# Optimization experiments

Hardware: AMD Instinct MI355X
Metric: run time of the kernel (lower is better)

Reference implementation:

```python
import jax, jax.numpy as jnp
import numpy as np

D_MODEL = 1024
N_HEADS = 16
D_FF = 2 * D_MODEL
EPS = 1e-6


def setup_inputs() -> dict:
    key = jax.random.key(0)
    ks = jax.random.split(key, 12)
    B, S, D = 2, 2048, D_MODEL
    w = lambda k, shape: (jax.random.normal(k, shape, dtype=jnp.float32) * 0.02)
    return {
        "x": jax.random.normal(ks[0], (B, S, D), dtype=jnp.float32),
        "mask": jnp.ones((B, S, S), dtype=jnp.int32),
        "alpha1": jnp.ones((D,), jnp.float32),
        "bias1": jnp.zeros((D,), jnp.float32),
        "Wq": w(ks[1], (D, D)), "bq": jnp.zeros((D,), jnp.float32),
        "Wk": w(ks[2], (D, D)), "bk": jnp.zeros((D,), jnp.float32),
        "Wv": w(ks[3], (D, D)), "bv": jnp.zeros((D,), jnp.float32),
        "Wo": w(ks[4], (D, D)), "bo": jnp.zeros((D,), jnp.float32),
        "alpha2": jnp.ones((D,), jnp.float32),
        "bias2": jnp.zeros((D,), jnp.float32),
        "W1": w(ks[5], (D, D_FF)), "b1": jnp.zeros((D_FF,), jnp.float32),
        "W2": w(ks[6], (D_FF, D)), "b2": jnp.zeros((D,), jnp.float32),
    }


def _norm(x, alpha, bias):
    # torch: alpha*(x-mean)/(std+eps)+bias, std is unbiased (ddof=1)
    mu = jnp.mean(x, axis=-1, keepdims=True)
    sd = jnp.std(x, axis=-1, ddof=1, keepdims=True)
    return alpha * (x - mu) / (sd + EPS) + bias


def _gelu(x):
    return jax.nn.gelu(x, approximate=False)  # torch F.gelu exact


def _attention(x2, mask, Wq, bq, Wk, bk, Wv, bv, Wo, bo):
    B, S, D = x2.shape
    h, dk = N_HEADS, D // N_HEADS
    # project and split heads: [B, h, S, dk]
    q = (x2 @ Wq + bq).reshape(B, S, h, dk).transpose(0, 2, 1, 3)
    k = (x2 @ Wk + bk).reshape(B, S, h, dk).transpose(0, 2, 1, 3)
    v = (x2 @ Wv + bv).reshape(B, S, h, dk).transpose(0, 2, 1, 3)
    scores = jnp.einsum('bhqd,bhkd->bhqk', q, k) / np.sqrt(dk).astype(np.float32)
    scores = jnp.where(mask[:, None] == 0, jnp.float32(-1e9), scores)
    attn = jax.nn.softmax(scores, axis=-1)
    out = jnp.einsum('bhqk,bhkd->bhqd', attn, v)
    out = out.transpose(0, 2, 1, 3).reshape(B, S, D)
    return out @ Wo + bo


def reference(x, mask, alpha1, bias1, Wq, bq, Wk, bk, Wv, bv, Wo, bo,
              alpha2, bias2, W1, b1, W2, b2):
    x2 = _norm(x, alpha1, bias1)
    x = x + _attention(x2, mask, Wq, bq, Wk, bk, Wv, bv, Wo, bo)
    x2 = _norm(x, alpha2, bias2)
    ff = _gelu(_gelu(x2 @ W1 + b1) @ W2 + b2)
    return x + ff
```

## Files before the change

### kernel.cpp

```cpp
#include <hip/hip_runtime.h>
#include <math.h>

typedef __attribute__((ext_vector_type(8))) short v8s;
typedef __attribute__((ext_vector_type(4))) float v4f;
typedef __attribute__((ext_vector_type(4))) unsigned int v4u;
typedef __attribute__((ext_vector_type(2))) unsigned int v2u;

#define MFMA16(a,b,c) __builtin_amdgcn_mfma_f32_16x16x32_bf16(a,b,c,0,0,0)
#define QSCALE 0.18033688011112042f

typedef const __attribute__((address_space(1))) void* gp1_t;
typedef __attribute__((address_space(3))) void* lp3_t;
__device__ __forceinline__ void gll16(const void* g, void* l){
  __builtin_amdgcn_global_load_lds((gp1_t)g, (lp3_t)l, 16, 0, 0);
}
#define VMCNT(n) asm volatile("s_waitcnt vmcnt(" #n ")" ::: "memory")

__device__ __forceinline__ unsigned short f2b(float f){
  unsigned u = __builtin_bit_cast(unsigned, f);
  u += 0x7FFFu + ((u>>16)&1u);
  return (unsigned short)(u>>16);
}
__device__ __forceinline__ unsigned cvtpk(float lo, float hi){
  unsigned r;
  asm("v_cvt_pk_bf16_f32 %0, %1, %2" : "=v"(r) : "v"(lo), "v"(hi));
  return r;
}
__device__ __forceinline__ float gelu_exact(float x){
  return 0.5f*x*(1.0f + erff(x*0.70710678118654752f));
}

__global__ __launch_bounds__(256) void ln_kernel(const float* __restrict__ x,
    const float* __restrict__ alpha, const float* __restrict__ bias,
    unsigned short* __restrict__ out)
{
  const int D = 1024;
  int row = blockIdx.x;
  int tid = threadIdx.x;
  const float* xr = x + (size_t)row*D;
  v4f v = ((const v4f*)xr)[tid];
  float s  = v[0]+v[1]+v[2]+v[3];
  float s2 = v[0]*v[0]+v[1]*v[1]+v[2]*v[2]+v[3]*v[3];
  #pragma unroll
  for (int off=1; off<64; off<<=1){ s += __shfl_xor(s, off); s2 += __shfl_xor(s2, off); }
  __shared__ float red[8];
  int w = tid>>6;
  if ((tid&63)==0){ red[w]=s; red[4+w]=s2; }
  __syncthreads();
  s  = red[0]+red[1]+red[2]+red[3];
  s2 = red[4]+red[5]+red[6]+red[7];
  float mu  = s*(1.0f/D);
  float var = (s2 - (float)D*mu*mu)*(1.0f/(D-1));
  float inv = 1.0f/(sqrtf(fmaxf(var,0.0f)) + 1e-6f);
  v4f a  = ((const v4f*)alpha)[tid];
  v4f bi = ((const v4f*)bias)[tid];
  unsigned short o[4];
  #pragma unroll
  for (int i=0;i<4;i++) o[i] = f2b(a[i]*(v[i]-mu)*inv + bi[i]);
  v2u pk; pk[0] = (unsigned)o[0] | ((unsigned)o[1]<<16);
          pk[1] = (unsigned)o[2] | ((unsigned)o[3]<<16);
  ((v2u*)(out + (size_t)row*D))[tid] = pk;
}

__global__ __launch_bounds__(256) void transpose_f2b(const float* __restrict__ in,
    unsigned short* __restrict__ out, int K, int N)
{
  __shared__ float t[32][33];
  int n0 = blockIdx.x*32, k0 = blockIdx.y*32;
  int tx = threadIdx.x, ty = threadIdx.y;
  #pragma unroll
  for (int j=0;j<4;j++) t[ty+8*j][tx] = in[(size_t)(k0+ty+8*j)*N + n0+tx];
  __syncthreads();
  #pragma unroll
  for (int j=0;j<4;j++) out[(size_t)(n0+ty+8*j)*K + k0+tx] = f2b(t[tx][ty+8*j]);
}

__global__ __launch_bounds__(256) void mask_flags(const int* __restrict__ mask,
    unsigned char* __restrict__ flags)
{
  const int S = 2048;
  int bid = blockIdx.x;
  int kt = bid & 31, qt = (bid>>5)&31, b = bid>>10;
  int tid = threadIdx.x;
  const int* mp = mask + (size_t)b*S*S + (size_t)(qt*64)*S + kt*64;
  int ok = 1;
  #pragma unroll
  for (int i=0;i<16;i++){
    int idx = tid + i*256;
    int row = idx>>6, col = idx&63;
    ok &= (mp[(size_t)row*S + col] != 0);
  }
  ok = __all(ok) ? 1 : 0;
  __shared__ int f[4];
  if ((tid&63)==0) f[tid>>6] = ok;
  __syncthreads();
  if (tid==0) flags[bid] = (unsigned char)(f[0]&f[1]&f[2]&f[3]);
}

__global__ __launch_bounds__(256) void v_transpose(const unsigned short* __restrict__ vB,
    unsigned short* __restrict__ vT)
{
  __shared__ unsigned short ts[64][68];
  int tt = blockIdx.x & 31, bh = blockIdx.x >> 5;
  int b = bh >> 4, h = bh & 15;
  int tid = threadIdx.x;
  int row = tid>>3, c8 = (tid&7)*8;
  const unsigned short* src = vB + ((size_t)(b*2048 + tt*64))*1024 + h*64;
  #pragma unroll
  for (int j=0;j<2;j++)
    *(v4u*)&ts[row+32*j][c8] = *(const v4u*)(src + (size_t)(row+32*j)*1024 + c8);
  __syncthreads();
  unsigned short* dst = vT + ((size_t)bh*64)*2048 + (size_t)tt*64;
  #pragma unroll
  for (int j=0;j<2;j++){
    int d = row + 32*j;
    unsigned short tmp[8];
    #pragma unroll
    for (int jj=0;jj<8;jj++) tmp[jj] = ts[c8+jj][d];
    *(v4u*)&dst[(size_t)d*2048 + c8] = *(const v4u*)tmp;
  }
}

__global__ __launch_bounds__(256) void gemm_qkv(
    const unsigned short* __restrict__ A, const unsigned short* __restrict__ Bt,
    const float* __restrict__ bq, const float* __restrict__ bk, const float* __restrict__ bv,
    unsigned short* __restrict__ qB, unsigned short* __restrict__ kB, unsigned short* __restrict__ vB)
{
  const int K = 1024, N = 1024;
  __shared__ unsigned short As[3][128][32];
  __shared__ unsigned short Bs[3][128][32];
  int m0 = blockIdx.x*128;
  int ny = blockIdx.y;
  int seg = ny>>3;
  int n0g = ny*128;
  int tid = threadIdx.x;
  int w = tid>>6, l = tid&63;
  int wm = (w>>1)*64, wn = (w&1)*64;
  int r16 = l&15, kq = l>>4;
  v4f acc[4][4] = {};
  int t4 = tid>>2, c8 = (tid&3)*8;
  const unsigned short* Ag = A  + (size_t)(m0 + t4)*K + c8;
  const unsigned short* Bg = Bt + (size_t)(n0g + t4)*K + c8;
  auto stageG = [&](int kb, int idx){
    char* a = (char*)&As[idx][0][0] + w*1024;
    char* b = (char*)&Bs[idx][0][0] + w*1024;
    gll16(Ag + kb,                a);
    gll16(Ag + (size_t)64*K + kb, a + 4096);
    gll16(Bg + kb,                b);
    gll16(Bg + (size_t)64*K + kb, b + 4096);
  };
  const int nk = K/32;
  stageG(0, 0); stageG(32, 1);
  for (int i=0; i<nk; i++){
    int cur = i%3;
    if (i+1 < nk) VMCNT(4); else VMCNT(0);
    __builtin_amdgcn_s_barrier();
    if (i+2 < nk) stageG((i+2)*32, (i+2)%3);
    v8s a[4], b[4];
    #pragma unroll
    for (int mi=0;mi<4;mi++) a[mi] = *(const v8s*)&As[cur][wm+mi*16+r16][kq*8];
    #pragma unroll
    for (int ni=0;ni<4;ni++) b[ni] = *(const v8s*)&Bs[cur][wn+ni*16+r16][kq*8];
    #pragma unroll
    for (int mi=0;mi<4;mi++)
      #pragma unroll
      for (int ni=0;ni<4;ni++)
        acc[mi][ni] = MFMA16(a[mi], b[ni], acc[mi][ni]);
  }
  unsigned short* ob = (seg==0) ? qB : (seg==1) ? kB : vB;
  const float*    bp = (seg==0) ? bq : (seg==1) ? bk : bv;
  float sc = (seg==0) ? QSCALE : 1.0f;
  int ncol0 = (ny&7)*128;
  #pragma unroll
  for (int mi=0;mi<4;mi++){
    #pragma unroll
    for (int ni=0;ni<4;ni++){
      int col = ncol0 + wn + ni*16 + r16;
      float bvv = bp[col];
      #pragma unroll
      for (int r=0;r<4;r++){
        int row = m0 + wm + mi*16 + kq*4 + r;
        ob[(size_t)row*N + col] = f2b((acc[mi][ni][r] + bvv)*sc);
      }
    }
  }
}

template<int MODE>
__global__ __launch_bounds__(256) void gemm_bt(
    const unsigned short* __restrict__ A, const unsigned short* __restrict__ Bt,
    const float* __restrict__ bias, const float* __restrict__ res,
    unsigned short* __restrict__ outb, float* __restrict__ outf,
    int M, int N, int K)
{
  __shared__ unsigned short As[3][128][32];
  __shared__ unsigned short Bs[3][128][32];
  int m0 = blockIdx.x*128, n0 = blockIdx.y*128;
  int tid = threadIdx.x;
  int w = tid>>6, l = tid&63;
  int wm = (w>>1)*64, wn = (w&1)*64;
  int r16 = l&15, kq = l>>4;
  v4f acc[4][4] = {};
  int t4 = tid>>2, c8 = (tid&3)*8;
  const unsigned short* Ag = A  + (size_t)(m0 + t4)*K + c8;
  const unsigned short* Bg = Bt + (size_t)(n0 + t4)*K + c8;
  auto stageG = [&](int kb, int idx){
    char* a = (char*)&As[idx][0][0] + w*1024;
    char* b = (char*)&Bs[idx][0][0] + w*1024;
    gll16(Ag + kb,                a);
    gll16(Ag + (size_t)64*K + kb, a + 4096);
    gll16(Bg + kb,                b);
    gll16(Bg + (size_t)64*K + kb, b + 4096);
  };
  const int nk = K/32;
  stageG(0, 0); stageG(32, 1);
  for (int i=0; i<nk; i++){
    int cur = i%3;
    if (i+1 < nk) VMCNT(4); else VMCNT(0);
    __builtin_amdgcn_s_barrier();
    if (i+2 < nk) stageG((i+2)*32, (i+2)%3);
    v8s a[4], b[4];
    #pragma unroll
    for (int mi=0;mi<4;mi++) a[mi] = *(const v8s*)&As[cur][wm+mi*16+r16][kq*8];
    #pragma unroll
    for (int ni=0;ni<4;ni++) b[ni] = *(const v8s*)&Bs[cur][wn+ni*16+r16][kq*8];
    #pragma unroll
    for (int mi=0;mi<4;mi++)
      #pragma unroll
      for (int ni=0;ni<4;ni++)
        acc[mi][ni] = MFMA16(a[mi], b[ni], acc[mi][ni]);
  }
  #pragma unroll
  for (int mi=0;mi<4;mi++){
    #pragma unroll
    for (int ni=0;ni<4;ni++){
      int col = n0 + wn + ni*16 + r16;
      float bv = bias[col];
      #pragma unroll
      for (int r=0;r<4;r++){
        int row = m0 + wm + mi*16 + kq*4 + r;
        float t = acc[mi][ni][r] + bv;
        if (MODE==2) t = gelu_exact(t);
        if (MODE==2) outb[(size_t)row*N + col] = f2b(t);
        else         outf[(size_t)row*N + col] = t + res[(size_t)row*N + col];
      }
    }
  }
}

template<int MODE>
__global__ __launch_bounds__(256) void gemm64_bt(
    const unsigned short* __restrict__ A, const unsigned short* __restrict__ Bt,
    const float* __restrict__ bias, const float* __restrict__ res,
    float* __restrict__ outf, int M, int N, int K)
{
  __shared__ unsigned short As[3][64][32];
  __shared__ unsigned short Bs[3][128][32];
  int m0 = blockIdx.x*64, n0 = blockIdx.y*128;
  int tid = threadIdx.x;
  int w = tid>>6, l = tid&63;
  int wm = (w>>1)*32, wn = (w&1)*64;
  int r16 = l&15, kq = l>>4;
  v4f acc[2][4] = {};
  int t4 = tid>>2, c8 = (tid&3)*8;
  const unsigned short* Ag = A  + (size_t)(m0 + t4)*K + c8;
  const unsigned short* Bg = Bt + (size_t)(n0 + t4)*K + c8;
  auto stageG = [&](int kb, int idx){
    char* a = (char*)&As[idx][0][0] + w*1024;
    char* b = (char*)&Bs[idx][0][0] + w*1024;
    gll16(Ag + kb,                a);
    gll16(Bg + kb,                b);
    gll16(Bg + (size_t)64*K + kb, b + 4096);
  };
  const int nk = K/32;
  stageG(0, 0); stageG(32, 1);
  for (int i=0; i<nk; i++){
    int cur = i%3;
    if (i+1 < nk) VMCNT(3); else VMCNT(0);
    __builtin_amdgcn_s_barrier();
    if (i+2 < nk) stageG((i+2)*32, (i+2)%3);
    v8s a[2], b[4];
    #pragma unroll
    for (int mi=0;mi<2;mi++) a[mi] = *(const v8s*)&As[cur][wm+mi*16+r16][kq*8];
    #pragma unroll
    for (int ni=0;ni<4;ni++) b[ni] = *(const v8s*)&Bs[cur][wn+ni*16+r16][kq*8];
    #pragma unroll
    for (int mi=0;mi<2;mi++)
      #pragma unroll
      for (int ni=0;ni<4;ni++)
        acc[mi][ni] = MFMA16(a[mi], b[ni], acc[mi][ni]);
  }
  #pragma unroll
  for (int mi=0;mi<2;mi++){
    #pragma unroll
    for (int ni=0;ni<4;ni++){
      int col = n0 + wn + ni*16 + r16;
      float bv = bias[col];
      #pragma unroll
      for (int r=0;r<4;r++){
        int row = m0 + wm + mi*16 + kq*4 + r;
        float t = acc[mi][ni][r] + bv;
        if (MODE==3) t = gelu_exact(t);
        outf[(size_t)row*N + col] = t + res[(size_t)row*N + col];
      }
    }
  }
}

__global__ __launch_bounds__(512, 4) void attn_kernel(
    const unsigned short* __restrict__ Q, const unsigned short* __restrict__ Kb,
    const unsigned short* __restrict__ vT, const int* __restrict__ mask,
    const unsigned char* __restrict__ flags, unsigned short* __restrict__ out)
{
  const int S = 2048, D = 1024;
  __shared__ unsigned short Kb3[3][64][64];
  __shared__ unsigned short Vb3[3][64][64];
  __shared__ unsigned short Ps[8][16][36];
  int bid = (blockIdx.x & 7)*64 + (blockIdx.x >> 3);
  int qt = bid & 15;
  int bh = bid >> 4;
  int b = bh >> 4, h = bh & 15;
  int tid = threadIdx.x, w = tid>>6, l = tid&63;
  int r16 = l&15, kq = l>>4;
  const unsigned short* Qp  = Q  + (size_t)b*S*D + h*64;
  const unsigned short* Kp  = Kb + (size_t)b*S*D + h*64;
  const unsigned short* vTp = vT + (size_t)bh*64*S;
  int qrow0 = qt*128 + w*16;
  v8s qf[2];
  #pragma unroll
  for (int ks=0;ks<2;ks++)
    qf[ks] = *(const v8s*)(Qp + (size_t)(qrow0+r16)*D + ks*32 + kq*8);
  float m_run = -1e30f, l_run = 0.0f;
  v4f o[4] = {};
  const int* mp = mask + (size_t)b*S*S;
  const unsigned char* fl = flags + ((size_t)b*32 + qt*2)*32;

  int srow = l>>3;
  int gsw  = (l&7) ^ srow;
  auto stage = [&](int kt, int idx){
    int kt64 = kt*64;
    int row = w*8 + srow;
    gll16(Kp  + (size_t)(kt64+row)*D + gsw*8, &Kb3[idx][w*8][0]);
    gll16(vTp + (size_t)row*S + kt64 + gsw*8, &Vb3[idx][w*8][0]);
  };

  stage(0, 0); stage(1, 1);
  for (int kt=0; kt<32; kt++){
    int cur = kt%3;
    if (kt+1 < 32) VMCNT(2); else VMCNT(0);
    __builtin_amdgcn_s_barrier();
    if (kt+2 < 32) stage(kt+2, (kt+2)%3);
    int kt64 = kt*64;
    int rx = r16 & 7;
    v4f s[4] = {};
    #pragma unroll
    for (int ks=0; ks<2; ks++){
      v8s kf[4];
      #pragma unroll
      for (int nj=0; nj<4; nj++)
        kf[nj] = *(const v8s*)&Kb3[cur][nj*16+r16][((ks*4+kq)^rx)*8];
      #pragma unroll
      for (int nj=0; nj<4; nj++)
        s[nj] = MFMA16(kf[nj], qf[ks], s[nj]);
    }
    if (!(fl[kt] & fl[32+kt])){
      int qrow = qrow0 + r16;
      #pragma unroll
      for (int nj=0;nj<4;nj++){
        #pragma unroll
        for (int r=0;r<4;r++){
          int kcol = kt64 + nj*16 + kq*4 + r;
          if (mp[(size_t)qrow*S + kcol] == 0) s[nj][r] = -3.0e38f;
        }
      }
    }
    float t0 = fmaxf(fmaxf(s[0][0],s[0][1]), fmaxf(s[0][2],s[0][3]));
    float t1 = fmaxf(fmaxf(s[1][0],s[1][1]), fmaxf(s[1][2],s[1][3]));
    float t2 = fmaxf(fmaxf(s[2][0],s[2][1]), fmaxf(s[2][2],s[2][3]));
    float t3 = fmaxf(fmaxf(s[3][0],s[3][1]), fmaxf(s[3][2],s[3][3]));
    float tm = fmaxf(fmaxf(t0,t1), fmaxf(t2,t3));
    tm = fmaxf(tm, __shfl_xor(tm,16));
    tm = fmaxf(tm, __shfl_xor(tm,32));
    if (!__all(tm <= m_run + 11.5f)){
      float mn = fmaxf(m_run, tm);
      float corr = exp2f(m_run - mn);
      m_run = mn;
      l_run *= corr;
      #pragma unroll
      for (int nj=0;nj<4;nj++)
        #pragma unroll
        for (int r=0;r<4;r++) o[nj][r] *= corr;
    }
    #pragma unroll
    for (int nj=0;nj<4;nj++)
      #pragma unroll
      for (int r=0;r<4;r++)
        s[nj][r] = exp2f(s[nj][r] - m_run);
    float a0 = (s[0][0]+s[0][1]) + (s[0][2]+s[0][3]);
    float a1 = (s[1][0]+s[1][1]) + (s[1][2]+s[1][3]);
    float a2 = (s[2][0]+s[2][1]) + (s[2][2]+s[2][3]);
    float a3 = (s[3][0]+s[3][1]) + (s[3][2]+s[3][3]);
    float rs = (a0+a1) + (a2+a3);
    rs += __shfl_xor(rs,16);
    rs += __shfl_xor(rs,32);
    l_run += rs;
    #pragma unroll
    for (int hh=0; hh<2; hh++){
      #pragma unroll
      for (int nj=hh*2; nj<hh*2+2; nj++){
        *(unsigned*)&Ps[w][r16][(nj&1)*16 + kq*4    ] = cvtpk(s[nj][0], s[nj][1]);
        *(unsigned*)&Ps[w][r16][(nj&1)*16 + kq*4 + 2] = cvtpk(s[nj][2], s[nj][3]);
      }
      v8s pa = *(const v8s*)&Ps[w][r16][kq*8];
      v8s vv[4];
      #pragma unroll
      for (int nj=0;nj<4;nj++)
        vv[nj] = *(const v8s*)&Vb3[cur][nj*16+r16][((hh*4+kq)^rx)*8];
      #pragma unroll
      for (int nj=0;nj<4;nj++)
        o[nj] = MFMA16(vv[nj], pa, o[nj]);
    }
  }
  float invl = 1.0f / l_run;
  size_t orow = (size_t)(b*S + qrow0 + r16)*D + h*64;
  #pragma unroll
  for (int nj=0;nj<4;nj++){
    v2u pk;
    pk[0] = cvtpk(o[nj][0]*invl, o[nj][1]*invl);
    pk[1] = cvtpk(o[nj][2]*invl, o[nj][3]*invl);
    *(v2u*)(out + orow + nj*16 + kq*4) = pk;
  }
}

extern "C" void kernel_launch(void* const* d_in, const int* in_sizes, int n_in,
                              void* d_out, int out_size, void* d_ws, size_t ws_size,
                              hipStream_t stream)
{
  const int D=1024, DFF=2048, BS=4096;
  const float* x      = (const float*)d_in[0];
  const int*   mask   = (const int*)d_in[1];
  const float* alpha1 = (const float*)d_in[2];
  const float* bias1  = (const float*)d_in[3];
  const float* Wq     = (const float*)d_in[4];
  const float* bq     = (const float*)d_in[5];
  const float* Wk     = (const float*)d_in[6];
  const float* bk     = (const float*)d_in[7];
  const float* Wv     = (const float*)d_in[8];
  const float* bv     = (const float*)d_in[9];
  const float* Wo     = (const float*)d_in[10];
  const float* bo     = (const float*)d_in[11];
  const float* alpha2 = (const float*)d_in[12];
  const float* bias2  = (const float*)d_in[13];
  const float* W1     = (const float*)d_in[14];
  const float* b1     = (const float*)d_in[15];
  const float* W2     = (const float*)d_in[16];
  const float* b2     = (const float*)d_in[17];
  float* outp = (float*)d_out;

  char* ws = (char*)d_ws;
  size_t off = 0;
  auto alloc = [&](size_t bytes){ void* p = ws+off; off += (bytes+255)&~(size_t)255; return p; };
  unsigned short* x2b    = (unsigned short*)alloc((size_t)BS*D*2);
  unsigned short* qB     = (unsigned short*)alloc((size_t)BS*D*2);
  unsigned short* kB     = (unsigned short*)alloc((size_t)BS*D*2);
  unsigned short* vB     = (unsigned short*)alloc((size_t)BS*D*2);
  unsigned short* attnB  = (unsigned short*)alloc((size_t)BS*D*2);
  unsigned short* h1     = (unsigned short*)alloc((size_t)BS*DFF*2);
  float*          xres   = (float*)alloc((size_t)BS*D*4);
  unsigned short* wqkvT  = (unsigned short*)alloc((size_t)3*D*D*2);
  unsigned short* woT    = (unsigned short*)alloc((size_t)D*D*2);
  unsigned short* w1T    = (unsigned short*)alloc((size_t)D*DFF*2);
  unsigned short* w2T    = (unsigned short*)alloc((size_t)DFF*D*2);
  unsigned char*  flg    = (unsigned char*)alloc(2048);
  unsigned short* vTb    = x2b;

  dim3 tb(32,8);
  transpose_f2b<<<dim3(D/32,  D/32 ), tb, 0, stream>>>(Wq, wqkvT,           D, D);
  transpose_f2b<<<dim3(D/32,  D/32 ), tb, 0, stream>>>(Wk, wqkvT + D*D,     D, D);
  transpose_f2b<<<dim3(D/32,  D/32 ), tb, 0, stream>>>(Wv, wqkvT + 2*D*D,   D, D);
  transpose_f2b<<<dim3(D/32,  D/32 ), tb, 0, stream>>>(Wo, woT, D, D);
  transpose_f2b<<<dim3(DFF/32,D/32 ), tb, 0, stream>>>(W1, w1T, D, DFF);
  transpose_f2b<<<dim3(D/32,  DFF/32), tb, 0, stream>>>(W2, w2T, DFF, D);

  mask_flags<<<2048, 256, 0, stream>>>(mask, flg);
  ln_kernel<<<BS, 256, 0, stream>>>(x, alpha1, bias1, x2b);

  gemm_qkv<<<dim3(BS/128, 24), 256, 0, stream>>>(x2b, wqkvT, bq, bk, bv, qB, kB, vB);

  v_transpose<<<1024, 256, 0, stream>>>(vB, vTb);

  attn_kernel<<<512, 512, 0, stream>>>(qB, kB, vTb, mask, flg, attnB);

  gemm64_bt<1><<<dim3(BS/64, D/128), 256, 0, stream>>>(attnB, woT, bo, x, xres, BS, D, D);

  ln_kernel<<<BS, 256, 0, stream>>>(xres, alpha2, bias2, x2b);

  gemm_bt<2><<<dim3(BS/128, DFF/128), 256, 0, stream>>>(x2b, w1T, b1, nullptr, h1, nullptr, BS, DFF, D);
  gemm64_bt<3><<<dim3(BS/64, D/128), 256, 0, stream>>>(h1, w2T, b2, xres, outp, BS, D, DFF);
}
```

Before: 259.3 us.

## Process two 16-row query tiles per wave in attention to reuse K/V fragments

The attention kernel now uses 256 threads (4 waves) per block, with each wave handling 32 query rows as two 16-row sub-tiles. Each K and V fragment read from LDS feeds two MFMAs, halving LDS traffic per FLOP, and each wave stages twice as many rows per tile. Per-tile mask-flag checks are precomputed once into a wave ballot bitmask instead of two global byte loads per iteration. The cost is higher register pressure (double accumulators and softmax state) and fewer waves per CU to hide latency.

```diff
diff --git a/kernel.cpp b/kernel.cpp
--- a/kernel.cpp
+++ b/kernel.cpp
@@ -307,7 +307,7 @@
   }
 }
 
-__global__ __launch_bounds__(512, 4) void attn_kernel(
+__global__ __launch_bounds__(256, 2) void attn_kernel(
     const unsigned short* __restrict__ Q, const unsigned short* __restrict__ Kb,
     const unsigned short* __restrict__ vT, const int* __restrict__ mask,
     const unsigned char* __restrict__ flags, unsigned short* __restrict__ out)
@@ -315,7 +315,7 @@
   const int S = 2048, D = 1024;
   __shared__ unsigned short Kb3[3][64][64];
   __shared__ unsigned short Vb3[3][64][64];
-  __shared__ unsigned short Ps[8][16][36];
+  __shared__ unsigned short Ps[4][2][16][36];
   int bid = (blockIdx.x & 7)*64 + (blockIdx.x >> 3);
   int qt = bid & 15;
   int bh = bid >> 4;
@@ -325,34 +325,39 @@
   const unsigned short* Qp  = Q  + (size_t)b*S*D + h*64;
   const unsigned short* Kp  = Kb + (size_t)b*S*D + h*64;
   const unsigned short* vTp = vT + (size_t)bh*64*S;
-  int qrow0 = qt*128 + w*16;
-  v8s qf[2];
-  #pragma unroll
-  for (int ks=0;ks<2;ks++)
-    qf[ks] = *(const v8s*)(Qp + (size_t)(qrow0+r16)*D + ks*32 + kq*8);
-  float m_run = -1e30f, l_run = 0.0f;
-  v4f o[4] = {};
+  int qrow0 = qt*128 + w*32;
+  v8s qf[2][2];
+  #pragma unroll
+  for (int mi=0;mi<2;mi++)
+    #pragma unroll
+    for (int ks=0;ks<2;ks++)
+      qf[mi][ks] = *(const v8s*)(Qp + (size_t)(qrow0+mi*16+r16)*D + ks*32 + kq*8);
+  float m_run[2] = {-1e30f, -1e30f}, l_run[2] = {0.0f, 0.0f};
+  v4f o[2][4] = {};
   const int* mp = mask + (size_t)b*S*S;
   const unsigned char* fl = flags + ((size_t)b*32 + qt*2)*32;
+  unsigned long long okmask = __ballot( l < 32 ? ((fl[l] & fl[32+l]) != 0) : 1 );
 
   int srow = l>>3;
   int gsw  = (l&7) ^ srow;
   auto stage = [&](int kt, int idx){
     int kt64 = kt*64;
-    int row = w*8 + srow;
-    gll16(Kp  + (size_t)(kt64+row)*D + gsw*8, &Kb3[idx][w*8][0]);
-    gll16(vTp + (size_t)row*S + kt64 + gsw*8, &Vb3[idx][w*8][0]);
+    #pragma unroll
+    for (int sub=0; sub<2; sub++){
+      int row = w*16 + sub*8 + srow;
+      gll16(Kp  + (size_t)(kt64+row)*D + gsw*8, &Kb3[idx][w*16+sub*8][0]);
+      gll16(vTp + (size_t)row*S + kt64 + gsw*8, &Vb3[idx][w*16+sub*8][0]);
+    }
   };
 
   stage(0, 0); stage(1, 1);
   for (int kt=0; kt<32; kt++){
     int cur = kt%3;
-    if (kt+1 < 32) VMCNT(2); else VMCNT(0);
+    if (kt+1 < 32) VMCNT(4); else VMCNT(0);
     __builtin_amdgcn_s_barrier();
     if (kt+2 < 32) stage(kt+2, (kt+2)%3);
-    int kt64 = kt*64;
     int rx = r16 & 7;
-    v4f s[4] = {};
+    v4f s[2][4] = {};
     #pragma unroll
     for (int ks=0; ks<2; ks++){
       v8s kf[4];
@@ -360,75 +365,91 @@
       for (int nj=0; nj<4; nj++)
         kf[nj] = *(const v8s*)&Kb3[cur][nj*16+r16][((ks*4+kq)^rx)*8];
       #pragma unroll
-      for (int nj=0; nj<4; nj++)
-        s[nj] = MFMA16(kf[nj], qf[ks], s[nj]);
-    }
-    if (!(fl[kt] & fl[32+kt])){
-      int qrow = qrow0 + r16;
-      #pragma unroll
-      for (int nj=0;nj<4;nj++){
+      for (int mi=0; mi<2; mi++)
         #pragma unroll
-        for (int r=0;r<4;r++){
-          int kcol = kt64 + nj*16 + kq*4 + r;
-          if (mp[(size_t)qrow*S + kcol] == 0) s[nj][r] = -3.0e38f;
-        }
+        for (int nj=0; nj<4; nj++)
+          s[mi][nj] = MFMA16(kf[nj], qf[mi][ks], s[mi][nj]);
+    }
+    if (((~okmask) >> kt) & 1ull){
+      int kt64 = kt*64;
+      #pragma unroll
+      for (int mi=0;mi<2;mi++){
+        int qrow = qrow0 + mi*16 + r16;
+        #pragma unroll
+        for (int nj=0;nj<4;nj++)
+          #pragma unroll
+          for (int r=0;r<4;r++){
+            int kcol = kt64 + nj*16 + kq*4 + r;
+            if (mp[(size_t)qrow*S + kcol] == 0) s[mi][nj][r] = -3.0e38f;
+          }
       }
     }
-    float t0 = fmaxf(fmaxf(s[0][0],s[0][1]), fmaxf(s[0][2],s[0][3]));
-    float t1 = fmaxf(fmaxf(s[1][0],s[1][1]), fmaxf(s[1][2],s[1][3]));
-    float t2 = fmaxf(fmaxf(s[2][0],s[2][1]), fmaxf(s[2][2],s[2][3]));
-    float t3 = fmaxf(fmaxf(s[3][0],s[3][1]), fmaxf(s[3][2],s[3][3]));
-    float tm = fmaxf(fmaxf(t0,t1), fmaxf(t2,t3));
-    tm = fmaxf(tm, __shfl_xor(tm,16));
-    tm = fmaxf(tm, __shfl_xor(tm,32));
-    if (!__all(tm <= m_run + 11.5f)){
-      float mn = fmaxf(m_run, tm);
-      float corr = exp2f(m_run - mn);
-      m_run = mn;
-      l_run *= corr;
+    #pragma unroll
+    for (int mi=0;mi<2;mi++){
+      float t0 = fmaxf(fmaxf(s[mi][0][0],s[mi][0][1]), fmaxf(s[mi][0][2],s[mi][0][3]));
+      float t1 = fmaxf(fmaxf(s[mi][1][0],s[mi][1][1]), fmaxf(s[mi][1][2],s[mi][1][3]));
+      float t2 = fmaxf(fmaxf(s[mi][2][0],s[mi][2][1]), fmaxf(s[mi][2][2],s[mi][2][3]));
+      float t3 = fmaxf(fmaxf(s[mi][3][0],s[mi][3][1]), fmaxf(s[mi][3][2],s[mi][3][3]));
+      float tm = fmaxf(fmaxf(t0,t1), fmaxf(t2,t3));
+      tm = fmaxf(tm, __shfl_xor(tm,16));
+      tm = fmaxf(tm, __shfl_xor(tm,32));
+      if (!__all(tm <= m_run[mi] + 11.5f)){
+        float mn = fmaxf(m_run[mi], tm);
+        float corr = exp2f(m_run[mi] - mn);
+        m_run[mi] = mn;
+        l_run[mi] *= corr;
+        #pragma unroll
+        for (int nj=0;nj<4;nj++)
+          #pragma unroll
+          for (int r=0;r<4;r++) o[mi][nj][r] *= corr;
+      }
       #pragma unroll
       for (int nj=0;nj<4;nj++)
         #pragma unroll
-        for (int r=0;r<4;r++) o[nj][r] *= corr;
-    }
-    #pragma unroll
-    for (int nj=0;nj<4;nj++)
-      #pragma unroll
-      for (int r=0;r<4;r++)
-        s[nj][r] = exp2f(s[nj][r] - m_run);
-    float a0 = (s[0][0]+s[0][1]) + (s[0][2]+s[0][3]);
-    float a1 = (s[1][0]+s[1][1]) + (s[1][2]+s[1][3]);
-    float a2 = (s[2][0]+s[2][1]) + (s[2][2]+s[2][3]);
-    float a3 = (s[3][0]+s[3][1]) + (s[3][2]+s[3][3]);
-    float rs = (a0+a1) + (a2+a3);
-    rs += __shfl_xor(rs,16);
-    rs += __shfl_xor(rs,32);
-    l_run += rs;
+        for (int r=0;r<4;r++)
+          s[mi][nj][r] = exp2f(s[mi][nj][r] - m_run[mi]);
+      float a0 = (s[mi][0][0]+s[mi][0][1]) + (s[mi][0][2]+s[mi][0][3]);
+      float a1 = (s[mi][1][0]+s[mi][1][1]) + (s[mi][1][2]+s[mi][1][3]);
+      float a2 = (s[mi][2][0]+s[mi][2][1]) + (s[mi][2][2]+s[mi][2][3]);
+      float a3 = (s[mi][3][0]+s[mi][3][1]) + (s[mi][3][2]+s[mi][3][3]);
+      float rs = (a0+a1) + (a2+a3);
+      rs += __shfl_xor(rs,16);
+      rs += __shfl_xor(rs,32);
+      l_run[mi] += rs;
+    }
     #pragma unroll
     for (int hh=0; hh<2; hh++){
       #pragma unroll
-      for (int nj=hh*2; nj<hh*2+2; nj++){
-        *(unsigned*)&Ps[w][r16][(nj&1)*16 + kq*4    ] = cvtpk(s[nj][0], s[nj][1]);
-        *(unsigned*)&Ps[w][r16][(nj&1)*16 + kq*4 + 2] = cvtpk(s[nj][2], s[nj][3]);
-      }
-      v8s pa = *(const v8s*)&Ps[w][r16][kq*8];
+      for (int mi=0;mi<2;mi++)
+        #pragma unroll
+        for (int nj=hh*2; nj<hh*2+2; nj++){
+          *(unsigned*)&Ps[w][mi][r16][(nj&1)*16 + kq*4    ] = cvtpk(s[mi][nj][0], s[mi][nj][1]);
+          *(unsigned*)&Ps[w][mi][r16][(nj&1)*16 + kq*4 + 2] = cvtpk(s[mi][nj][2], s[mi][nj][3]);
+        }
       v8s vv[4];
       #pragma unroll
       for (int nj=0;nj<4;nj++)
         vv[nj] = *(const v8s*)&Vb3[cur][nj*16+r16][((hh*4+kq)^rx)*8];
       #pragma unroll
-      for (int nj=0;nj<4;nj++)
-        o[nj] = MFMA16(vv[nj], pa, o[nj]);
-    }
-  }
-  float invl = 1.0f / l_run;
-  size_t orow = (size_t)(b*S + qrow0 + r16)*D + h*64;
-  #pragma unroll
-  for (int nj=0;nj<4;nj++){
-    v2u pk;
-    pk[0] = cvtpk(o[nj][0]*invl, o[nj][1]*invl);
-    pk[1] = cvtpk(o[nj][2]*invl, o[nj][3]*invl);
-    *(v2u*)(out + orow + nj*16 + kq*4) = pk;
+      for (int mi=0;mi<2;mi++){
+        v8s pa = *(const v8s*)&Ps[w][mi][r16][kq*8];
+        #pragma unroll
+        for (int nj=0;nj<4;nj++)
+          o[mi][nj] = MFMA16(vv[nj], pa, o[mi][nj]);
+      }
+    }
+  }
+  #pragma unroll
+  for (int mi=0;mi<2;mi++){
+    float invl = 1.0f / l_run[mi];
+    size_t orow = (size_t)(b*S + qrow0 + mi*16 + r16)*D + h*64;
+    #pragma unroll
+    for (int nj=0;nj<4;nj++){
+      v2u pk;
+      pk[0] = cvtpk(o[mi][nj][0]*invl, o[mi][nj][1]*invl);
+      pk[1] = cvtpk(o[mi][nj][2]*invl, o[mi][nj][3]*invl);
+      *(v2u*)(out + orow + nj*16 + kq*4) = pk;
+    }
   }
 }
 
@@ -489,7 +510,7 @@
 
   v_transpose<<<1024, 256, 0, stream>>>(vB, vTb);
 
-  attn_kernel<<<512, 512, 0, stream>>>(qB, kB, vTb, mask, flg, attnB);
+  attn_kernel<<<512, 256, 0, stream>>>(qB, kB, vTb, mask, flg, attnB);
 
   gemm64_bt<1><<<dim3(BS/64, D/128), 256, 0, stream>>>(attnB, woT, bo, x, xres, BS, D, D);
 
```

Result: slower. 265.9 us (+2.6%).

## Switch attention to 32x32x16 MFMA with 4 waves of 32 query rows

Applied to the files above, without the earlier changes.

The flash-attention kernel now uses 4 waves, each owning 32 query rows, and issues 32x32x16 bf16 MFMAs instead of 16x16x32. With this layout the row max and row sum need one cross-lane shuffle instead of two, and each wave stages twice as many K/V rows. Mask-tile flags are precomputed once into a ballot bitmask, and s_setprio is raised around the MFMA sections. The block shrinks to 256 threads, so fewer waves are available per CU to hide latency, and the larger accumulators add register pressure.

```diff
diff --git a/kernel.cpp b/kernel.cpp
--- a/kernel.cpp
+++ b/kernel.cpp
@@ -3,10 +3,12 @@
 
 typedef __attribute__((ext_vector_type(8))) short v8s;
 typedef __attribute__((ext_vector_type(4))) float v4f;
+typedef __attribute__((ext_vector_type(16))) float v16f;
 typedef __attribute__((ext_vector_type(4))) unsigned int v4u;
 typedef __attribute__((ext_vector_type(2))) unsigned int v2u;
 
 #define MFMA16(a,b,c) __builtin_amdgcn_mfma_f32_16x16x32_bf16(a,b,c,0,0,0)
+#define MFMA32(a,b,c) __builtin_amdgcn_mfma_f32_32x32x16_bf16(a,b,c,0,0,0)
 #define QSCALE 0.18033688011112042f
 
 typedef const __attribute__((address_space(1))) void* gp1_t;
@@ -307,7 +309,7 @@
   }
 }
 
-__global__ __launch_bounds__(512, 4) void attn_kernel(
+__global__ __launch_bounds__(256, 2) void attn_kernel(
     const unsigned short* __restrict__ Q, const unsigned short* __restrict__ Kb,
     const unsigned short* __restrict__ vT, const int* __restrict__ mask,
     const unsigned char* __restrict__ flags, unsigned short* __restrict__ out)
@@ -315,120 +317,119 @@
   const int S = 2048, D = 1024;
   __shared__ unsigned short Kb3[3][64][64];
   __shared__ unsigned short Vb3[3][64][64];
-  __shared__ unsigned short Ps[8][16][36];
+  __shared__ unsigned short Ps[4][32][66];
   int bid = (blockIdx.x & 7)*64 + (blockIdx.x >> 3);
   int qt = bid & 15;
   int bh = bid >> 4;
   int b = bh >> 4, h = bh & 15;
   int tid = threadIdx.x, w = tid>>6, l = tid&63;
-  int r16 = l&15, kq = l>>4;
+  int l31 = l & 31, hi = l >> 5;
   const unsigned short* Qp  = Q  + (size_t)b*S*D + h*64;
   const unsigned short* Kp  = Kb + (size_t)b*S*D + h*64;
   const unsigned short* vTp = vT + (size_t)bh*64*S;
-  int qrow0 = qt*128 + w*16;
-  v8s qf[2];
-  #pragma unroll
-  for (int ks=0;ks<2;ks++)
-    qf[ks] = *(const v8s*)(Qp + (size_t)(qrow0+r16)*D + ks*32 + kq*8);
+  int qrow0 = qt*128 + w*32;
+  int qrow  = qrow0 + l31;
+  v8s qfr[4];
+  #pragma unroll
+  for (int ks=0;ks<4;ks++)
+    qfr[ks] = *(const v8s*)(Qp + (size_t)qrow*D + ks*16 + hi*8);
   float m_run = -1e30f, l_run = 0.0f;
-  v4f o[4] = {};
+  v16f o0 = {}, o1 = {};
   const int* mp = mask + (size_t)b*S*S;
   const unsigned char* fl = flags + ((size_t)b*32 + qt*2)*32;
+  unsigned long long okmask = __ballot( l < 32 ? ((fl[l] & fl[32+l]) != 0) : 1 );
 
   int srow = l>>3;
   int gsw  = (l&7) ^ srow;
   auto stage = [&](int kt, int idx){
     int kt64 = kt*64;
-    int row = w*8 + srow;
-    gll16(Kp  + (size_t)(kt64+row)*D + gsw*8, &Kb3[idx][w*8][0]);
-    gll16(vTp + (size_t)row*S + kt64 + gsw*8, &Vb3[idx][w*8][0]);
+    #pragma unroll
+    for (int sub=0; sub<2; sub++){
+      int row = w*16 + sub*8 + srow;
+      gll16(Kp  + (size_t)(kt64+row)*D + gsw*8, &Kb3[idx][w*16+sub*8][0]);
+      gll16(vTp + (size_t)row*S + kt64 + gsw*8, &Vb3[idx][w*16+sub*8][0]);
+    }
   };
 
   stage(0, 0); stage(1, 1);
   for (int kt=0; kt<32; kt++){
     int cur = kt%3;
-    if (kt+1 < 32) VMCNT(2); else VMCNT(0);
+    if (kt+1 < 32) VMCNT(4); else VMCNT(0);
     __builtin_amdgcn_s_barrier();
     if (kt+2 < 32) stage(kt+2, (kt+2)%3);
-    int kt64 = kt*64;
-    int rx = r16 & 7;
-    v4f s[4] = {};
-    #pragma unroll
-    for (int ks=0; ks<2; ks++){
-      v8s kf[4];
-      #pragma unroll
-      for (int nj=0; nj<4; nj++)
-        kf[nj] = *(const v8s*)&Kb3[cur][nj*16+r16][((ks*4+kq)^rx)*8];
-      #pragma unroll
-      for (int nj=0; nj<4; nj++)
-        s[nj] = MFMA16(kf[nj], qf[ks], s[nj]);
-    }
-    if (!(fl[kt] & fl[32+kt])){
-      int qrow = qrow0 + r16;
-      #pragma unroll
-      for (int nj=0;nj<4;nj++){
-        #pragma unroll
-        for (int r=0;r<4;r++){
-          int kcol = kt64 + nj*16 + kq*4 + r;
-          if (mp[(size_t)qrow*S + kcol] == 0) s[nj][r] = -3.0e38f;
-        }
+    int l7 = l & 7;
+    v16f s0 = {}, s1 = {};
+    __builtin_amdgcn_s_setprio(1);
+    #pragma unroll
+    for (int ks=0; ks<4; ks++){
+      v8s kf0 = *(const v8s*)&Kb3[cur][l31     ][(((ks*2) + hi) ^ l7)*8];
+      v8s kf1 = *(const v8s*)&Kb3[cur][32 + l31][(((ks*2) + hi) ^ l7)*8];
+      s0 = MFMA32(kf0, qfr[ks], s0);
+      s1 = MFMA32(kf1, qfr[ks], s1);
+    }
+    __builtin_amdgcn_s_setprio(0);
+    if (((~okmask) >> kt) & 1ull){
+      #pragma unroll
+      for (int r=0;r<16;r++){
+        int kvl = (r&3) + 8*(r>>2) + 4*hi;
+        if (mp[(size_t)qrow*S + kt*64 + kvl]      == 0) s0[r] = -3.0e38f;
+        if (mp[(size_t)qrow*S + kt*64 + 32 + kvl] == 0) s1[r] = -3.0e38f;
       }
     }
-    float t0 = fmaxf(fmaxf(s[0][0],s[0][1]), fmaxf(s[0][2],s[0][3]));
-    float t1 = fmaxf(fmaxf(s[1][0],s[1][1]), fmaxf(s[1][2],s[1][3]));
-    float t2 = fmaxf(fmaxf(s[2][0],s[2][1]), fmaxf(s[2][2],s[2][3]));
-    float t3 = fmaxf(fmaxf(s[3][0],s[3][1]), fmaxf(s[3][2],s[3][3]));
+    float t0 = fmaxf(fmaxf(fmaxf(s0[0],s0[1]),fmaxf(s0[2],s0[3])),
+                     fmaxf(fmaxf(s0[4],s0[5]),fmaxf(s0[6],s0[7])));
+    float t1 = fmaxf(fmaxf(fmaxf(s0[8],s0[9]),fmaxf(s0[10],s0[11])),
+                     fmaxf(fmaxf(s0[12],s0[13]),fmaxf(s0[14],s0[15])));
+    float t2 = fmaxf(fmaxf(fmaxf(s1[0],s1[1]),fmaxf(s1[2],s1[3])),
+                     fmaxf(fmaxf(s1[4],s1[5]),fmaxf(s1[6],s1[7])));
+    float t3 = fmaxf(fmaxf(fmaxf(s1[8],s1[9]),fmaxf(s1[10],s1[11])),
+                     fmaxf(fmaxf(s1[12],s1[13]),fmaxf(s1[14],s1[15])));
     float tm = fmaxf(fmaxf(t0,t1), fmaxf(t2,t3));
-    tm = fmaxf(tm, __shfl_xor(tm,16));
-    tm = fmaxf(tm, __shfl_xor(tm,32));
+    tm = fmaxf(tm, __shfl_xor(tm, 32));
     if (!__all(tm <= m_run + 11.5f)){
       float mn = fmaxf(m_run, tm);
       float corr = exp2f(m_run - mn);
       m_run = mn;
       l_run *= corr;
       #pragma unroll
-      for (int nj=0;nj<4;nj++)
-        #pragma unroll
-        for (int r=0;r<4;r++) o[nj][r] *= corr;
-    }
-    #pragma unroll
-    for (int nj=0;nj<4;nj++)
-      #pragma unroll
-      for (int r=0;r<4;r++)
-        s[nj][r] = exp2f(s[nj][r] - m_run);
-    float a0 = (s[0][0]+s[0][1]) + (s[0][2]+s[0][3]);
-    float a1 = (s[1][0]+s[1][1]) + (s[1][2]+s[1][3]);
-    float a2 = (s[2][0]+s[2][1]) + (s[2][2]+s[2][3]);
-    float a3 = (s[3][0]+s[3][1]) + (s[3][2]+s[3][3]);
+      for (int r=0;r<16;r++){ o0[r] *= corr; o1[r] *= corr; }
+    }
+    #pragma unroll
+    for (int r=0;r<16;r++){
+      s0[r] = exp2f(s0[r] - m_run);
+      s1[r] = exp2f(s1[r] - m_run);
+    }
+    float a0 = ((s0[0]+s0[1])+(s0[2]+s0[3])) + ((s0[4]+s0[5])+(s0[6]+s0[7]));
+    float a1 = ((s0[8]+s0[9])+(s0[10]+s0[11])) + ((s0[12]+s0[13])+(s0[14]+s0[15]));
+    float a2 = ((s1[0]+s1[1])+(s1[2]+s1[3])) + ((s1[4]+s1[5])+(s1[6]+s1[7]));
+    float a3 = ((s1[8]+s1[9])+(s1[10]+s1[11])) + ((s1[12]+s1[13])+(s1[14]+s1[15]));
     float rs = (a0+a1) + (a2+a3);
-    rs += __shfl_xor(rs,16);
-    rs += __shfl_xor(rs,32);
+    rs += __shfl_xor(rs, 32);
     l_run += rs;
     #pragma unroll
-    for (int hh=0; hh<2; hh++){
-      #pragma unroll
-      for (int nj=hh*2; nj<hh*2+2; nj++){
-        *(unsigned*)&Ps[w][r16][(nj&1)*16 + kq*4    ] = cvtpk(s[nj][0], s[nj][1]);
-        *(unsigned*)&Ps[w][r16][(nj&1)*16 + kq*4 + 2] = cvtpk(s[nj][2], s[nj][3]);
-      }
-      v8s pa = *(const v8s*)&Ps[w][r16][kq*8];
-      v8s vv[4];
-      #pragma unroll
-      for (int nj=0;nj<4;nj++)
-        vv[nj] = *(const v8s*)&Vb3[cur][nj*16+r16][((hh*4+kq)^rx)*8];
-      #pragma unroll
-      for (int nj=0;nj<4;nj++)
-        o[nj] = MFMA16(vv[nj], pa, o[nj]);
-    }
+    for (int p=0; p<8; p++){
+      int kvb = (p&1)*2 + 8*(p>>1) + 4*hi;
+      *(unsigned*)&Ps[w][l31][kvb]      = cvtpk(s0[2*p], s0[2*p+1]);
+      *(unsigned*)&Ps[w][l31][32 + kvb] = cvtpk(s1[2*p], s1[2*p+1]);
+    }
+    __builtin_amdgcn_s_setprio(1);
+    #pragma unroll
+    for (int kvs=0; kvs<4; kvs++){
+      v8s pb  = *(const v8s*)&Ps[w][l31][kvs*16 + hi*8];
+      v8s vv0 = *(const v8s*)&Vb3[cur][l31     ][(((kvs*2) + hi) ^ l7)*8];
+      v8s vv1 = *(const v8s*)&Vb3[cur][32 + l31][(((kvs*2) + hi) ^ l7)*8];
+      o0 = MFMA32(vv0, pb, o0);
+      o1 = MFMA32(vv1, pb, o1);
+    }
+    __builtin_amdgcn_s_setprio(0);
   }
   float invl = 1.0f / l_run;
-  size_t orow = (size_t)(b*S + qrow0 + r16)*D + h*64;
-  #pragma unroll
-  for (int nj=0;nj<4;nj++){
-    v2u pk;
-    pk[0] = cvtpk(o[nj][0]*invl, o[nj][1]*invl);
-    pk[1] = cvtpk(o[nj][2]*invl, o[nj][3]*invl);
-    *(v2u*)(out + orow + nj*16 + kq*4) = pk;
+  size_t obase = (size_t)(b*S + qrow)*D + h*64;
+  #pragma unroll
+  for (int p=0; p<8; p++){
+    int dk = (p&1)*2 + 8*(p>>1) + 4*hi;
+    *(unsigned*)(out + obase + dk)      = cvtpk(o0[2*p]*invl, o0[2*p+1]*invl);
+    *(unsigned*)(out + obase + 32 + dk) = cvtpk(o1[2*p]*invl, o1[2*p+1]*invl);
   }
 }
 
@@ -489,7 +490,7 @@
 
   v_transpose<<<1024, 256, 0, stream>>>(vB, vTb);
 
-  attn_kernel<<<512, 512, 0, stream>>>(qB, kB, vTb, mask, flg, attnB);
+  attn_kernel<<<512, 256, 0, stream>>>(qB, kB, vTb, mask, flg, attnB);
 
   gemm64_bt<1><<<dim3(BS/64, D/128), 256, 0, stream>>>(attnB, woT, bo, x, xres, BS, D, D);
 
```

Measured after the change: 260.4 us. Within noise of the previous version (+0.5%).
